# Kernel tuning notes

Measured on AMD Instinct MI355X. Metric: run time of the kernel, lower is better.

Reference implementation:

```python
import jax, jax.numpy as jnp
import numpy as np

N_NODES = 50000
N_EDGES = 600000
D_IN = 128
D_HID = 128


def _gcn_layer(x, src, dst, W, b, n):
    # PyG GCNConv: h = x @ W; add self-loops; symmetric normalization
    # out_i = sum_j (d_i^-1/2 d_j^-1/2) h_j + (d_i^-1) h_i + b, with d = deg + 1
    h = x @ W  # [N, F]
    ones = jnp.ones(src.shape[0], dtype=x.dtype)
    deg = jax.ops.segment_sum(ones, dst, num_segments=n) + jnp.asarray(1.0, x.dtype)
    dinv = jax.lax.rsqrt(deg)  # [N]
    coef = dinv[src] * dinv[dst]  # [E]
    msg = h[src] * coef[:, None]  # gather + scale, [E, F]
    agg = jax.ops.segment_sum(msg, dst, num_segments=n)  # scatter-add, [N, F]
    agg = agg + h * (dinv * dinv)[:, None]  # self-loop contribution
    return agg + b


def setup_inputs() -> dict:
    key = jax.random.key(0)
    k1, k2, k3, k4 = jax.random.split(key, 4)
    x = jax.random.normal(k1, (N_NODES, D_IN), dtype=jnp.float32)
    edge_index = jax.random.randint(k2, (2, N_EDGES), 0, N_NODES, dtype=jnp.int32)
    # Glorot-ish init for linear weights
    W1 = jax.random.normal(k3, (D_IN, D_HID), dtype=jnp.float32) / np.sqrt(D_IN)
    W2 = jax.random.normal(k4, (D_HID, D_HID), dtype=jnp.float32) / np.sqrt(D_HID)
    b1 = jnp.zeros((D_HID,), dtype=jnp.float32)
    b2 = jnp.zeros((D_HID,), dtype=jnp.float32)
    return {"x": x, "edge_index": edge_index, "W1": W1, "b1": b1, "W2": W2, "b2": b2}


def reference(x, edge_index, W1, b1, W2, b2):
    src = edge_index[0]
    dst = edge_index[1]
    n = x.shape[0]
    h = _gcn_layer(x, src, dst, W1, b1, n)
    h = jax.nn.relu(h)
    out = _gcn_layer(h, src, dst, W2, b2, n)
    return out
```

## Files before the change

### kernel.cpp

```cpp
#include <hip/hip_runtime.h>
#include <hip/hip_bf16.h>

typedef __attribute__((ext_vector_type(8))) short short8;
typedef __attribute__((ext_vector_type(4))) float floatx4;

#define D 128
#define BCAP 2048
#define CPAD 16

__device__ __forceinline__ unsigned short f2bf(float f) {
    unsigned u = __float_as_uint(f);
    u += 0x7FFFu + ((u >> 16) & 1u);
    return (unsigned short)(u >> 16);
}
__device__ __forceinline__ float bf2f(unsigned short h) {
    return __uint_as_float(((unsigned)h) << 16);
}
__device__ __forceinline__ float bflo(unsigned p) { return __uint_as_float(p << 16); }
__device__ __forceinline__ float bfhi(unsigned p) { return __uint_as_float(p & 0xFFFF0000u); }

__global__ __launch_bounds__(256) void bucket_wconv_kernel(const int* __restrict__ src,
                                                           const int* __restrict__ dst,
                                                           int* __restrict__ bcnt,
                                                           unsigned* __restrict__ bucket, int E,
                                                           const float* __restrict__ W1,
                                                           const float* __restrict__ W2,
                                                           unsigned short* __restrict__ whi1,
                                                           unsigned short* __restrict__ wlo1,
                                                           unsigned short* __restrict__ whi2,
                                                           unsigned short* __restrict__ wlo2,
                                                           int eb4) {
    int b = blockIdx.x;
    if (b >= eb4) {
        int gid = (b - eb4) * 256 + threadIdx.x;
        int which = gid >> 14;
        int tid = gid & 16383;
        const float* W = which ? W2 : W1;
        unsigned short* whi = which ? whi2 : whi1;
        unsigned short* wlo = which ? wlo2 : wlo1;
        int j    = tid & 7;
        int col  = (tid >> 3) & 127;
        int quad = (tid >> 10) & 3;
        int kb   = tid >> 12;
        float wv = W[(kb * 32 + quad * 8 + j) * D + col];
        unsigned u = __float_as_uint(wv);
        unsigned short h = (unsigned short)(u >> 16);
        whi[tid] = h;
        wlo[tid] = f2bf(wv - bf2f(h));
        return;
    }
    int sub = b & 7;
    int t4 = (b * 256 + threadIdx.x) * 4;
    if (t4 + 3 < E) {
        int4 s = *reinterpret_cast<const int4*>(src + t4);
        int4 d = *reinterpret_cast<const int4*>(dst + t4);
        #pragma unroll
        for (int k = 0; k < 4; k++) {
            int dd = (k == 0) ? d.x : (k == 1) ? d.y : (k == 2) ? d.z : d.w;
            int ss = (k == 0) ? s.x : (k == 1) ? s.y : (k == 2) ? s.z : s.w;
            int slot = ((dd >> 8) << 3) | sub;
            int pos = atomicAdd(&bcnt[slot * CPAD], 1);
            if (pos < BCAP)
                bucket[(size_t)slot * BCAP + pos] = ((unsigned)(dd & 255) << 16) | (unsigned)ss;
        }
    } else {
        for (int i = t4; i < E; i++) {
            int dd = dst[i], ss = src[i];
            int slot = ((dd >> 8) << 3) | sub;
            int pos = atomicAdd(&bcnt[slot * CPAD], 1);
            if (pos < BCAP)
                bucket[(size_t)slot * BCAP + pos] = ((unsigned)(dd & 255) << 16) | (unsigned)ss;
        }
    }
}

__device__ __forceinline__ int block_excl_scan256(int v, int* lds, int tid) {
    int lane = tid & 63, wid = tid >> 6;
    int x = v;
    #pragma unroll
    for (int d = 1; d < 64; d <<= 1) {
        int y = __shfl_up(x, d, 64);
        if (lane >= d) x += y;
    }
    if (lane == 63) lds[wid] = x;
    __syncthreads();
    if (tid == 0) {
        int run = 0;
        #pragma unroll
        for (int i = 0; i < 4; i++) { int t2 = lds[i]; lds[i] = run; run += t2; }
    }
    __syncthreads();
    return lds[wid] + x - v;
}

__global__ __launch_bounds__(256) void build_gemm_kernel(const unsigned* __restrict__ bucket,
                                                         const int* __restrict__ bcnt,
                                                         int* __restrict__ row_ptr,
                                                         float* __restrict__ dinv,
                                                         int* __restrict__ esrc, int N, int E,
                                                         const float* __restrict__ A,
                                                         const unsigned short* __restrict__ whi,
                                                         const unsigned short* __restrict__ wlo,
                                                         unsigned short* __restrict__ C, int M,
                                                         int nbuk) {
    __shared__ int lds4[4];
    __shared__ int sbase[256];
    __shared__ int hist[256];
    __shared__ int cur[256];
    int tid = threadIdx.x;
    int b = blockIdx.x;
    if (b < nbuk) {
        int tot = 0;
        if (tid < nbuk) {
            #pragma unroll
            for (int s = 0; s < 8; s++) tot += min(bcnt[(tid * 8 + s) * CPAD], BCAP);
        }
        int ex = block_excl_scan256(tot, lds4, tid);
        sbase[tid] = ex;
        hist[tid] = 0;
        __syncthreads();
        int base = sbase[b];
        for (int sub = 0; sub < 8; sub++) {
            int cnt = min(bcnt[(b * 8 + sub) * CPAD], BCAP);
            const unsigned* bp = bucket + (size_t)(b * 8 + sub) * BCAP;
            for (int i = tid; i < cnt; i += 256)
                atomicAdd(&hist[bp[i] >> 16], 1);
        }
        __syncthreads();
        int h = hist[tid];
        int off = block_excl_scan256(h, lds4, tid);
        cur[tid] = base + off;
        int node = b * 256 + tid;
        if (node < N) {
            row_ptr[node] = base + off;
            dinv[node] = rsqrtf((float)(h + 1));
        }
        if (b == 0 && tid == 0) row_ptr[N] = E;
        __syncthreads();
        for (int sub = 0; sub < 8; sub++) {
            int cnt = min(bcnt[(b * 8 + sub) * CPAD], BCAP);
            const unsigned* bp = bucket + (size_t)(b * 8 + sub) * BCAP;
            for (int i = tid; i < cnt; i += 256) {
                unsigned v = bp[i];
                int p = atomicAdd(&cur[v >> 16], 1);
                esrc[p] = (int)(v & 0xFFFFu);
            }
        }
        return;
    }
    int lane = tid & 63, wid = tid >> 6;
    int quad = lane >> 4, l15 = lane & 15;
    int row0 = (b - nbuk) * 64;
    int n0 = wid * 32;

    short8 bhi[2][4], blo[2][4];
    #pragma unroll
    for (int t = 0; t < 2; t++)
        #pragma unroll
        for (int kb = 0; kb < 4; kb++) {
            size_t base = ((size_t)((kb * 4 + quad) * 128 + (n0 + t * 16 + l15))) * 8;
            bhi[t][kb] = *reinterpret_cast<const short8*>(whi + base);
            blo[t][kb] = *reinterpret_cast<const short8*>(wlo + base);
        }

    #pragma unroll
    for (int rg = 0; rg < 4; rg++) {
        int r0 = row0 + rg * 16;
        int ar = r0 + l15; if (ar > M - 1) ar = M - 1;
        short8 ahi[4], alo[4];
        #pragma unroll
        for (int kb = 0; kb < 4; kb++) {
            const float4* ap = reinterpret_cast<const float4*>(A + (size_t)ar * D + kb * 32 + quad * 8);
            float4 v0 = ap[0], v1 = ap[1];
            float vv[8] = {v0.x, v0.y, v0.z, v0.w, v1.x, v1.y, v1.z, v1.w};
            short8 vh, vl;
            #pragma unroll
            for (int j = 0; j < 8; j++) {
                unsigned u = __float_as_uint(vv[j]);
                unsigned short h = (unsigned short)(u >> 16);
                vh[j] = (short)h;
                vl[j] = (short)f2bf(vv[j] - bf2f(h));
            }
            ahi[kb] = vh;
            alo[kb] = vl;
        }
        floatx4 acc0 = {0.f, 0.f, 0.f, 0.f};
        floatx4 acc1 = {0.f, 0.f, 0.f, 0.f};
        #pragma unroll
        for (int kb = 0; kb < 4; kb++) {
            acc0 = __builtin_amdgcn_mfma_f32_16x16x32_bf16(ahi[kb], bhi[0][kb], acc0, 0, 0, 0);
            acc1 = __builtin_amdgcn_mfma_f32_16x16x32_bf16(ahi[kb], bhi[1][kb], acc1, 0, 0, 0);
            acc0 = __builtin_amdgcn_mfma_f32_16x16x32_bf16(ahi[kb], blo[0][kb], acc0, 0, 0, 0);
            acc1 = __builtin_amdgcn_mfma_f32_16x16x32_bf16(ahi[kb], blo[1][kb], acc1, 0, 0, 0);
            acc0 = __builtin_amdgcn_mfma_f32_16x16x32_bf16(alo[kb], bhi[0][kb], acc0, 0, 0, 0);
            acc1 = __builtin_amdgcn_mfma_f32_16x16x32_bf16(alo[kb], bhi[1][kb], acc1, 0, 0, 0);
        }
        #pragma unroll
        for (int r = 0; r < 4; r++) {
            int orow = r0 + quad * 4 + r;
            if (orow < M) {
                C[(size_t)orow * D + n0 + l15]      = f2bf(acc0[r]);
                C[(size_t)orow * D + n0 + 16 + l15] = f2bf(acc1[r]);
            }
        }
    }
}

__device__ __forceinline__ void agg_qbody(const uint4* __restrict__ H4,
                                          const float* __restrict__ dinv,
                                          const int* __restrict__ row_ptr,
                                          const int* __restrict__ esrc,
                                          const float* __restrict__ bias,
                                          int node, int fl, float* acc) {
    #pragma unroll
    for (int j = 0; j < 8; j++) acc[j] = 0.f;
    int beg = row_ptr[node], end = row_ptr[node + 1];
    int e = beg;
    for (; e + 4 <= end; e += 4) {
        int s0 = esrc[e], s1 = esrc[e + 1], s2 = esrc[e + 2], s3 = esrc[e + 3];
        float c0 = dinv[s0], c1 = dinv[s1], c2 = dinv[s2], c3 = dinv[s3];
        uint4 p0 = H4[(size_t)s0 * 16 + fl];
        uint4 p1 = H4[(size_t)s1 * 16 + fl];
        uint4 p2 = H4[(size_t)s2 * 16 + fl];
        uint4 p3 = H4[(size_t)s3 * 16 + fl];
        acc[0] += c0 * bflo(p0.x) + c1 * bflo(p1.x) + c2 * bflo(p2.x) + c3 * bflo(p3.x);
        acc[1] += c0 * bfhi(p0.x) + c1 * bfhi(p1.x) + c2 * bfhi(p2.x) + c3 * bfhi(p3.x);
        acc[2] += c0 * bflo(p0.y) + c1 * bflo(p1.y) + c2 * bflo(p2.y) + c3 * bflo(p3.y);
        acc[3] += c0 * bfhi(p0.y) + c1 * bfhi(p1.y) + c2 * bfhi(p2.y) + c3 * bfhi(p3.y);
        acc[4] += c0 * bflo(p0.z) + c1 * bflo(p1.z) + c2 * bflo(p2.z) + c3 * bflo(p3.z);
        acc[5] += c0 * bfhi(p0.z) + c1 * bfhi(p1.z) + c2 * bfhi(p2.z) + c3 * bfhi(p3.z);
        acc[6] += c0 * bflo(p0.w) + c1 * bflo(p1.w) + c2 * bflo(p2.w) + c3 * bflo(p3.w);
        acc[7] += c0 * bfhi(p0.w) + c1 * bfhi(p1.w) + c2 * bfhi(p2.w) + c3 * bfhi(p3.w);
    }
    for (; e < end; e++) {
        int s0 = esrc[e];
        float c = dinv[s0];
        uint4 p0 = H4[(size_t)s0 * 16 + fl];
        acc[0] += c * bflo(p0.x); acc[1] += c * bfhi(p0.x);
        acc[2] += c * bflo(p0.y); acc[3] += c * bfhi(p0.y);
        acc[4] += c * bflo(p0.z); acc[5] += c * bfhi(p0.z);
        acc[6] += c * bflo(p0.w); acc[7] += c * bfhi(p0.w);
    }
    float di = dinv[node];
    float dii = di * di;
    uint4 ps = H4[(size_t)node * 16 + fl];
    const float4* b4 = (const float4*)bias;
    float4 bb0 = b4[fl * 2], bb1 = b4[fl * 2 + 1];
    #pragma unroll
    for (int j = 0; j < 8; j++) acc[j] *= di;
    acc[0] += dii * bflo(ps.x) + bb0.x;
    acc[1] += dii * bfhi(ps.x) + bb0.y;
    acc[2] += dii * bflo(ps.y) + bb0.z;
    acc[3] += dii * bfhi(ps.y) + bb0.w;
    acc[4] += dii * bflo(ps.z) + bb1.x;
    acc[5] += dii * bfhi(ps.z) + bb1.y;
    acc[6] += dii * bflo(ps.w) + bb1.z;
    acc[7] += dii * bfhi(ps.w) + bb1.w;
}

__global__ __launch_bounds__(256) void agg_gemm2_kernel(const unsigned short* __restrict__ H,
                                                        const float* __restrict__ dinv,
                                                        const int* __restrict__ row_ptr,
                                                        const int* __restrict__ esrc,
                                                        const float* __restrict__ bias,
                                                        const unsigned short* __restrict__ whi,
                                                        const unsigned short* __restrict__ wlo,
                                                        unsigned short* __restrict__ C, int N) {
    __shared__ unsigned short Asm[16 * 136];
    int tid = threadIdx.x;
    int node0 = blockIdx.x * 16;
    int r = tid >> 4;
    int fl = tid & 15;
    int node = node0 + r;
    float acc[8];
    if (node < N) {
        agg_qbody((const uint4*)H, dinv, row_ptr, esrc, bias, node, fl, acc);
    } else {
        #pragma unroll
        for (int j = 0; j < 8; j++) acc[j] = 0.f;
    }
    short8 a;
    #pragma unroll
    for (int j = 0; j < 8; j++) a[j] = (short)f2bf(fmaxf(acc[j], 0.f));
    *reinterpret_cast<short8*>(&Asm[r * 136 + fl * 8]) = a;
    __syncthreads();

    int lane = tid & 63, wid = tid >> 6;
    int quad = lane >> 4, l15 = lane & 15;
    int n0 = wid * 32;
    floatx4 acc0 = {0.f, 0.f, 0.f, 0.f};
    floatx4 acc1 = {0.f, 0.f, 0.f, 0.f};
    #pragma unroll 1
    for (int kb = 0; kb < 4; kb++) {
        size_t wb = ((size_t)((kb * 4 + quad) * 128 + (n0 + l15))) * 8;
        short8 bh0 = *reinterpret_cast<const short8*>(whi + wb);
        short8 bh1 = *reinterpret_cast<const short8*>(whi + wb + 128);
        short8 bl0 = *reinterpret_cast<const short8*>(wlo + wb);
        short8 bl1 = *reinterpret_cast<const short8*>(wlo + wb + 128);
        short8 af = *reinterpret_cast<const short8*>(&Asm[l15 * 136 + kb * 32 + quad * 8]);
        acc0 = __builtin_amdgcn_mfma_f32_16x16x32_bf16(af, bh0, acc0, 0, 0, 0);
        acc1 = __builtin_amdgcn_mfma_f32_16x16x32_bf16(af, bh1, acc1, 0, 0, 0);
        acc0 = __builtin_amdgcn_mfma_f32_16x16x32_bf16(af, bl0, acc0, 0, 0, 0);
        acc1 = __builtin_amdgcn_mfma_f32_16x16x32_bf16(af, bl1, acc1, 0, 0, 0);
    }
    #pragma unroll
    for (int rr = 0; rr < 4; rr++) {
        int orow = node0 + quad * 4 + rr;
        if (orow < N) {
            C[(size_t)orow * D + n0 + l15]      = f2bf(acc0[rr]);
            C[(size_t)orow * D + n0 + 16 + l15] = f2bf(acc1[rr]);
        }
    }
}

__global__ __launch_bounds__(256) void agg_f32out_kernel(const unsigned short* __restrict__ H,
                                                         const float* __restrict__ dinv,
                                                         const int* __restrict__ row_ptr,
                                                         const int* __restrict__ esrc,
                                                         const float* __restrict__ bias,
                                                         float4* __restrict__ out, int N) {
    int node = blockIdx.x * 16 + (threadIdx.x >> 4);
    int fl = threadIdx.x & 15;
    if (node >= N) return;
    float acc[8];
    agg_qbody((const uint4*)H, dinv, row_ptr, esrc, bias, node, fl, acc);
    float4 o0, o1;
    o0.x = acc[0]; o0.y = acc[1]; o0.z = acc[2]; o0.w = acc[3];
    o1.x = acc[4]; o1.y = acc[5]; o1.z = acc[6]; o1.w = acc[7];
    out[(size_t)node * 32 + fl * 2]     = o0;
    out[(size_t)node * 32 + fl * 2 + 1] = o1;
}

extern "C" void kernel_launch(void* const* d_in, const int* in_sizes, int n_in,
                              void* d_out, int out_size, void* d_ws, size_t ws_size,
                              hipStream_t stream) {
    const float* x  = (const float*)d_in[0];
    const int*   ei = (const int*)d_in[1];
    const float* W1 = (const float*)d_in[2];
    const float* b1 = (const float*)d_in[3];
    const float* W2 = (const float*)d_in[4];
    const float* b2 = (const float*)d_in[5];

    int N = in_sizes[0] / D;
    int E = in_sizes[1] / 2;
    const int* src = ei;
    const int* dst = ei + E;

    int nbuk = (N + 255) / 256;

    char* ws = (char*)d_ws;
    int*      bcnt   = (int*)(ws + 0);
    unsigned* bucket = (unsigned*)(ws + 102400);
    int*      row_ptr= (int*)(ws + 12947456);
    float*    dinv   = (float*)(ws + 13147520);
    int*      esrcs  = (int*)(ws + 13347520);
    unsigned short* whi1 = (unsigned short*)(ws + 15747584);
    unsigned short* wlo1 = (unsigned short*)(ws + 15780352);
    unsigned short* whi2 = (unsigned short*)(ws + 15813120);
    unsigned short* wlo2 = (unsigned short*)(ws + 15845888);
    unsigned short* hfeat = (unsigned short*)(ws + 15878656);
    unsigned short* h2    = (unsigned short*)(ws + 28678656);

    int eb4  = (E / 4 + 255) / 256;
    int gb   = (N + 63) / 64;
    int ab16 = (N + 15) / 16;

    hipMemsetAsync(bcnt, 0, (size_t)nbuk * 8 * CPAD * sizeof(int), stream);
    bucket_wconv_kernel<<<eb4 + 128, 256, 0, stream>>>(src, dst, bcnt, bucket, E,
                                                       W1, W2, whi1, wlo1, whi2, wlo2, eb4);

    build_gemm_kernel<<<nbuk + gb, 256, 0, stream>>>(bucket, bcnt, row_ptr, dinv, esrcs,
                                                     N, E, x, whi1, wlo1, hfeat, N, nbuk);

    agg_gemm2_kernel<<<ab16, 256, 0, stream>>>(hfeat, dinv, row_ptr, esrcs, b1,
                                               whi2, wlo2, h2, N);

    agg_f32out_kernel<<<ab16, 256, 0, stream>>>(h2, dinv, row_ptr, esrcs, b2,
                                                (float4*)d_out, N);
}
```

Baseline: 192.4 us.

## Compute degrees in bucketing pass and pack source coefficient into CSR edges

Per-node in-degrees are now counted with global atomics during edge bucketing, replacing the LDS histogram pass over buckets in the CSR build. The CSR edge array becomes (src, dinv[src]) pairs, so the aggregation kernels no longer do a dependent gather of dinv per edge. The aggregation inner loop is also unrolled to 8 edges to keep more feature loads in flight. The cost is an extra global atomic per edge, a random deg read per edge during the build, and a doubled edge array footprint.

```diff
diff --git a/kernel.cpp b/kernel.cpp
--- a/kernel.cpp
+++ b/kernel.cpp
@@ -22,6 +22,7 @@
 __global__ __launch_bounds__(256) void bucket_wconv_kernel(const int* __restrict__ src,
                                                            const int* __restrict__ dst,
                                                            int* __restrict__ bcnt,
+                                                           int* __restrict__ deg,
                                                            unsigned* __restrict__ bucket, int E,
                                                            const float* __restrict__ W1,
                                                            const float* __restrict__ W2,
@@ -59,6 +60,7 @@
             int dd = (k == 0) ? d.x : (k == 1) ? d.y : (k == 2) ? d.z : d.w;
             int ss = (k == 0) ? s.x : (k == 1) ? s.y : (k == 2) ? s.z : s.w;
             int slot = ((dd >> 8) << 3) | sub;
+            atomicAdd(&deg[dd], 1);
             int pos = atomicAdd(&bcnt[slot * CPAD], 1);
             if (pos < BCAP)
                 bucket[(size_t)slot * BCAP + pos] = ((unsigned)(dd & 255) << 16) | (unsigned)ss;
@@ -67,6 +69,7 @@
         for (int i = t4; i < E; i++) {
             int dd = dst[i], ss = src[i];
             int slot = ((dd >> 8) << 3) | sub;
+            atomicAdd(&deg[dd], 1);
             int pos = atomicAdd(&bcnt[slot * CPAD], 1);
             if (pos < BCAP)
                 bucket[(size_t)slot * BCAP + pos] = ((unsigned)(dd & 255) << 16) | (unsigned)ss;
@@ -95,9 +98,10 @@
 
 __global__ __launch_bounds__(256) void build_gemm_kernel(const unsigned* __restrict__ bucket,
                                                          const int* __restrict__ bcnt,
+                                                         const int* __restrict__ deg,
                                                          int* __restrict__ row_ptr,
                                                          float* __restrict__ dinv,
-                                                         int* __restrict__ esrc, int N, int E,
+                                                         uint2* __restrict__ edata, int N, int E,
                                                          const float* __restrict__ A,
                                                          const unsigned short* __restrict__ whi,
                                                          const unsigned short* __restrict__ wlo,
@@ -105,7 +109,6 @@
                                                          int nbuk) {
     __shared__ int lds4[4];
     __shared__ int sbase[256];
-    __shared__ int hist[256];
     __shared__ int cur[256];
     int tid = threadIdx.x;
     int b = blockIdx.x;
@@ -117,20 +120,12 @@
         }
         int ex = block_excl_scan256(tot, lds4, tid);
         sbase[tid] = ex;
-        hist[tid] = 0;
         __syncthreads();
         int base = sbase[b];
-        for (int sub = 0; sub < 8; sub++) {
-            int cnt = min(bcnt[(b * 8 + sub) * CPAD], BCAP);
-            const unsigned* bp = bucket + (size_t)(b * 8 + sub) * BCAP;
-            for (int i = tid; i < cnt; i += 256)
-                atomicAdd(&hist[bp[i] >> 16], 1);
-        }
-        __syncthreads();
-        int h = hist[tid];
+        int node = b * 256 + tid;
+        int h = (node < N) ? deg[node] : 0;
         int off = block_excl_scan256(h, lds4, tid);
         cur[tid] = base + off;
-        int node = b * 256 + tid;
         if (node < N) {
             row_ptr[node] = base + off;
             dinv[node] = rsqrtf((float)(h + 1));
@@ -142,8 +137,11 @@
             const unsigned* bp = bucket + (size_t)(b * 8 + sub) * BCAP;
             for (int i = tid; i < cnt; i += 256) {
                 unsigned v = bp[i];
+                int ss = (int)(v & 0xFFFFu);
                 int p = atomicAdd(&cur[v >> 16], 1);
-                esrc[p] = (int)(v & 0xFFFFu);
+                float cs = rsqrtf((float)(deg[ss] + 1));
+                uint2 ent; ent.x = (unsigned)ss; ent.y = __float_as_uint(cs);
+                edata[p] = ent;
             }
         }
         return;
@@ -206,36 +204,59 @@
     }
 }
 
+#define ACC4(c0, p0, c1, p1, c2, p2, c3, p3) \
+    acc[0] += c0 * bflo(p0.x) + c1 * bflo(p1.x) + c2 * bflo(p2.x) + c3 * bflo(p3.x); \
+    acc[1] += c0 * bfhi(p0.x) + c1 * bfhi(p1.x) + c2 * bfhi(p2.x) + c3 * bfhi(p3.x); \
+    acc[2] += c0 * bflo(p0.y) + c1 * bflo(p1.y) + c2 * bflo(p2.y) + c3 * bflo(p3.y); \
+    acc[3] += c0 * bfhi(p0.y) + c1 * bfhi(p1.y) + c2 * bfhi(p2.y) + c3 * bfhi(p3.y); \
+    acc[4] += c0 * bflo(p0.z) + c1 * bflo(p1.z) + c2 * bflo(p2.z) + c3 * bflo(p3.z); \
+    acc[5] += c0 * bfhi(p0.z) + c1 * bfhi(p1.z) + c2 * bfhi(p2.z) + c3 * bfhi(p3.z); \
+    acc[6] += c0 * bflo(p0.w) + c1 * bflo(p1.w) + c2 * bflo(p2.w) + c3 * bflo(p3.w); \
+    acc[7] += c0 * bfhi(p0.w) + c1 * bfhi(p1.w) + c2 * bfhi(p2.w) + c3 * bfhi(p3.w);
+
 __device__ __forceinline__ void agg_qbody(const uint4* __restrict__ H4,
+                                          const uint2* __restrict__ ed,
                                           const float* __restrict__ dinv,
                                           const int* __restrict__ row_ptr,
-                                          const int* __restrict__ esrc,
                                           const float* __restrict__ bias,
                                           int node, int fl, float* acc) {
     #pragma unroll
     for (int j = 0; j < 8; j++) acc[j] = 0.f;
     int beg = row_ptr[node], end = row_ptr[node + 1];
     int e = beg;
-    for (; e + 4 <= end; e += 4) {
-        int s0 = esrc[e], s1 = esrc[e + 1], s2 = esrc[e + 2], s3 = esrc[e + 3];
-        float c0 = dinv[s0], c1 = dinv[s1], c2 = dinv[s2], c3 = dinv[s3];
-        uint4 p0 = H4[(size_t)s0 * 16 + fl];
-        uint4 p1 = H4[(size_t)s1 * 16 + fl];
-        uint4 p2 = H4[(size_t)s2 * 16 + fl];
-        uint4 p3 = H4[(size_t)s3 * 16 + fl];
-        acc[0] += c0 * bflo(p0.x) + c1 * bflo(p1.x) + c2 * bflo(p2.x) + c3 * bflo(p3.x);
-        acc[1] += c0 * bfhi(p0.x) + c1 * bfhi(p1.x) + c2 * bfhi(p2.x) + c3 * bfhi(p3.x);
-        acc[2] += c0 * bflo(p0.y) + c1 * bflo(p1.y) + c2 * bflo(p2.y) + c3 * bflo(p3.y);
-        acc[3] += c0 * bfhi(p0.y) + c1 * bfhi(p1.y) + c2 * bfhi(p2.y) + c3 * bfhi(p3.y);
-        acc[4] += c0 * bflo(p0.z) + c1 * bflo(p1.z) + c2 * bflo(p2.z) + c3 * bflo(p3.z);
-        acc[5] += c0 * bfhi(p0.z) + c1 * bfhi(p1.z) + c2 * bfhi(p2.z) + c3 * bfhi(p3.z);
-        acc[6] += c0 * bflo(p0.w) + c1 * bflo(p1.w) + c2 * bflo(p2.w) + c3 * bflo(p3.w);
-        acc[7] += c0 * bfhi(p0.w) + c1 * bfhi(p1.w) + c2 * bfhi(p2.w) + c3 * bfhi(p3.w);
+    for (; e + 8 <= end; e += 8) {
+        uint2 q0 = ed[e],     q1 = ed[e + 1], q2 = ed[e + 2], q3 = ed[e + 3];
+        uint2 q4 = ed[e + 4], q5 = ed[e + 5], q6 = ed[e + 6], q7 = ed[e + 7];
+        uint4 p0 = H4[(size_t)q0.x * 16 + fl];
+        uint4 p1 = H4[(size_t)q1.x * 16 + fl];
+        uint4 p2 = H4[(size_t)q2.x * 16 + fl];
+        uint4 p3 = H4[(size_t)q3.x * 16 + fl];
+        uint4 p4 = H4[(size_t)q4.x * 16 + fl];
+        uint4 p5 = H4[(size_t)q5.x * 16 + fl];
+        uint4 p6 = H4[(size_t)q6.x * 16 + fl];
+        uint4 p7 = H4[(size_t)q7.x * 16 + fl];
+        float c0 = __uint_as_float(q0.y), c1 = __uint_as_float(q1.y);
+        float c2 = __uint_as_float(q2.y), c3 = __uint_as_float(q3.y);
+        float c4 = __uint_as_float(q4.y), c5 = __uint_as_float(q5.y);
+        float c6 = __uint_as_float(q6.y), c7 = __uint_as_float(q7.y);
+        ACC4(c0, p0, c1, p1, c2, p2, c3, p3);
+        ACC4(c4, p4, c5, p5, c6, p6, c7, p7);
+    }
+    if (e + 4 <= end) {
+        uint2 q0 = ed[e], q1 = ed[e + 1], q2 = ed[e + 2], q3 = ed[e + 3];
+        uint4 p0 = H4[(size_t)q0.x * 16 + fl];
+        uint4 p1 = H4[(size_t)q1.x * 16 + fl];
+        uint4 p2 = H4[(size_t)q2.x * 16 + fl];
+        uint4 p3 = H4[(size_t)q3.x * 16 + fl];
+        float c0 = __uint_as_float(q0.y), c1 = __uint_as_float(q1.y);
+        float c2 = __uint_as_float(q2.y), c3 = __uint_as_float(q3.y);
+        ACC4(c0, p0, c1, p1, c2, p2, c3, p3);
+        e += 4;
     }
     for (; e < end; e++) {
-        int s0 = esrc[e];
-        float c = dinv[s0];
-        uint4 p0 = H4[(size_t)s0 * 16 + fl];
+        uint2 q0 = ed[e];
+        float c = __uint_as_float(q0.y);
+        uint4 p0 = H4[(size_t)q0.x * 16 + fl];
         acc[0] += c * bflo(p0.x); acc[1] += c * bfhi(p0.x);
         acc[2] += c * bflo(p0.y); acc[3] += c * bfhi(p0.y);
         acc[4] += c * bflo(p0.z); acc[5] += c * bfhi(p0.z);
@@ -259,9 +280,9 @@
 }
 
 __global__ __launch_bounds__(256) void agg_gemm2_kernel(const unsigned short* __restrict__ H,
+                                                        const uint2* __restrict__ ed,
                                                         const float* __restrict__ dinv,
                                                         const int* __restrict__ row_ptr,
-                                                        const int* __restrict__ esrc,
                                                         const float* __restrict__ bias,
                                                         const unsigned short* __restrict__ whi,
                                                         const unsigned short* __restrict__ wlo,
@@ -274,7 +295,7 @@
     int node = node0 + r;
     float acc[8];
     if (node < N) {
-        agg_qbody((const uint4*)H, dinv, row_ptr, esrc, bias, node, fl, acc);
+        agg_qbody((const uint4*)H, ed, dinv, row_ptr, bias, node, fl, acc);
     } else {
         #pragma unroll
         for (int j = 0; j < 8; j++) acc[j] = 0.f;
@@ -314,16 +335,16 @@
 }
 
 __global__ __launch_bounds__(256) void agg_f32out_kernel(const unsigned short* __restrict__ H,
+                                                         const uint2* __restrict__ ed,
                                                          const float* __restrict__ dinv,
                                                          const int* __restrict__ row_ptr,
-                                                         const int* __restrict__ esrc,
                                                          const float* __restrict__ bias,
                                                          float4* __restrict__ out, int N) {
     int node = blockIdx.x * 16 + (threadIdx.x >> 4);
     int fl = threadIdx.x & 15;
     if (node >= N) return;
     float acc[8];
-    agg_qbody((const uint4*)H, dinv, row_ptr, esrc, bias, node, fl, acc);
+    agg_qbody((const uint4*)H, ed, dinv, row_ptr, bias, node, fl, acc);
     float4 o0, o1;
     o0.x = acc[0]; o0.y = acc[1]; o0.z = acc[2]; o0.w = acc[3];
     o1.x = acc[4]; o1.y = acc[5]; o1.z = acc[6]; o1.w = acc[7];
@@ -350,31 +371,32 @@
 
     char* ws = (char*)d_ws;
     int*      bcnt   = (int*)(ws + 0);
-    unsigned* bucket = (unsigned*)(ws + 102400);
-    int*      row_ptr= (int*)(ws + 12947456);
-    float*    dinv   = (float*)(ws + 13147520);
-    int*      esrcs  = (int*)(ws + 13347520);
-    unsigned short* whi1 = (unsigned short*)(ws + 15747584);
-    unsigned short* wlo1 = (unsigned short*)(ws + 15780352);
-    unsigned short* whi2 = (unsigned short*)(ws + 15813120);
-    unsigned short* wlo2 = (unsigned short*)(ws + 15845888);
-    unsigned short* hfeat = (unsigned short*)(ws + 15878656);
-    unsigned short* h2    = (unsigned short*)(ws + 28678656);
+    int*      deg    = (int*)(ws + 102400);
+    unsigned* bucket = (unsigned*)(ws + 307200);
+    int*      row_ptr= (int*)(ws + 13152256);
+    float*    dinv   = (float*)(ws + 13357056);
+    uint2*    edata  = (uint2*)(ws + 13561856);
+    unsigned short* whi1 = (unsigned short*)(ws + 18366464);
+    unsigned short* wlo1 = (unsigned short*)(ws + 18399232);
+    unsigned short* whi2 = (unsigned short*)(ws + 18432000);
+    unsigned short* wlo2 = (unsigned short*)(ws + 18464768);
+    unsigned short* hfeat = (unsigned short*)(ws + 18497536);
+    unsigned short* h2    = (unsigned short*)(ws + 31297536);
 
     int eb4  = (E / 4 + 255) / 256;
     int gb   = (N + 63) / 64;
     int ab16 = (N + 15) / 16;
 
-    hipMemsetAsync(bcnt, 0, (size_t)nbuk * 8 * CPAD * sizeof(int), stream);
-    bucket_wconv_kernel<<<eb4 + 128, 256, 0, stream>>>(src, dst, bcnt, bucket, E,
+    hipMemsetAsync(bcnt, 0, 307200, stream);
+    bucket_wconv_kernel<<<eb4 + 128, 256, 0, stream>>>(src, dst, bcnt, deg, bucket, E,
                                                        W1, W2, whi1, wlo1, whi2, wlo2, eb4);
 
-    build_gemm_kernel<<<nbuk + gb, 256, 0, stream>>>(bucket, bcnt, row_ptr, dinv, esrcs,
+    build_gemm_kernel<<<nbuk + gb, 256, 0, stream>>>(bucket, bcnt, deg, row_ptr, dinv, edata,
                                                      N, E, x, whi1, wlo1, hfeat, N, nbuk);
 
-    agg_gemm2_kernel<<<ab16, 256, 0, stream>>>(hfeat, dinv, row_ptr, esrcs, b1,
+    agg_gemm2_kernel<<<ab16, 256, 0, stream>>>(hfeat, edata, dinv, row_ptr, b1,
                                                whi2, wlo2, h2, N);
 
-    agg_f32out_kernel<<<ab16, 256, 0, stream>>>(h2, dinv, row_ptr, esrcs, b2,
+    agg_f32out_kernel<<<ab16, 256, 0, stream>>>(h2, edata, dinv, row_ptr, b2,
                                                 (float4*)d_out, N);
 }
```

Measured after the change: 222.8 us. 15.8% more time.

## Bin edges locally in LDS before scattering into global buckets

Applied to the files above, without the earlier changes.

The edge-bucketing pass now uses 256 blocks that each take a contiguous chunk of edges. Each block builds a shared-memory histogram by destination bucket and does a counting sort in LDS. It then reserves space with one global atomic per bucket and writes the sorted entries out. This replaces one global atomic per edge and scattered writes with aggregated atomics and more contiguous stores, at the cost of large LDS use and fewer blocks.

```diff
diff --git a/kernel.cpp b/kernel.cpp
--- a/kernel.cpp
+++ b/kernel.cpp
@@ -7,6 +7,8 @@
 #define D 128
 #define BCAP 2048
 #define CPAD 16
+#define NBIN 256
+#define EPBMAX 2560
 
 __device__ __forceinline__ unsigned short f2bf(float f) {
     unsigned u = __float_as_uint(f);
@@ -18,6 +20,25 @@
 }
 __device__ __forceinline__ float bflo(unsigned p) { return __uint_as_float(p << 16); }
 __device__ __forceinline__ float bfhi(unsigned p) { return __uint_as_float(p & 0xFFFF0000u); }
+
+__device__ __forceinline__ int block_excl_scan256(int v, int* lds, int tid) {
+    int lane = tid & 63, wid = tid >> 6;
+    int x = v;
+    #pragma unroll
+    for (int d = 1; d < 64; d <<= 1) {
+        int y = __shfl_up(x, d, 64);
+        if (lane >= d) x += y;
+    }
+    if (lane == 63) lds[wid] = x;
+    __syncthreads();
+    if (tid == 0) {
+        int run = 0;
+        #pragma unroll
+        for (int i = 0; i < 4; i++) { int t2 = lds[i]; lds[i] = run; run += t2; }
+    }
+    __syncthreads();
+    return lds[wid] + x - v;
+}
 
 __global__ __launch_bounds__(256) void bucket_wconv_kernel(const int* __restrict__ src,
                                                            const int* __restrict__ dst,
@@ -29,10 +50,10 @@
                                                            unsigned short* __restrict__ wlo1,
                                                            unsigned short* __restrict__ whi2,
                                                            unsigned short* __restrict__ wlo2,
-                                                           int eb4) {
+                                                           int nbuk) {
     int b = blockIdx.x;
-    if (b >= eb4) {
-        int gid = (b - eb4) * 256 + threadIdx.x;
+    if (b >= NBIN) {
+        int gid = (b - NBIN) * 256 + threadIdx.x;
         int which = gid >> 14;
         int tid = gid & 16383;
         const float* W = which ? W2 : W1;
@@ -49,48 +70,57 @@
         wlo[tid] = f2bf(wv - bf2f(h));
         return;
     }
+    __shared__ unsigned lent[EPBMAX];
+    __shared__ unsigned sorted_e[EPBMAX];
+    __shared__ int sdst[EPBMAX];
+    __shared__ unsigned short loff[EPBMAX];
+    __shared__ unsigned char lbkt[EPBMAX];
+    __shared__ int hist[256];
+    __shared__ int lstart[256];
+    __shared__ int gbase[256];
+    __shared__ int lds4[4];
+
+    int tid = threadIdx.x;
     int sub = b & 7;
-    int t4 = (b * 256 + threadIdx.x) * 4;
-    if (t4 + 3 < E) {
-        int4 s = *reinterpret_cast<const int4*>(src + t4);
-        int4 d = *reinterpret_cast<const int4*>(dst + t4);
-        #pragma unroll
-        for (int k = 0; k < 4; k++) {
-            int dd = (k == 0) ? d.x : (k == 1) ? d.y : (k == 2) ? d.z : d.w;
-            int ss = (k == 0) ? s.x : (k == 1) ? s.y : (k == 2) ? s.z : s.w;
-            int slot = ((dd >> 8) << 3) | sub;
-            int pos = atomicAdd(&bcnt[slot * CPAD], 1);
-            if (pos < BCAP)
-                bucket[(size_t)slot * BCAP + pos] = ((unsigned)(dd & 255) << 16) | (unsigned)ss;
-        }
-    } else {
-        for (int i = t4; i < E; i++) {
-            int dd = dst[i], ss = src[i];
-            int slot = ((dd >> 8) << 3) | sub;
-            int pos = atomicAdd(&bcnt[slot * CPAD], 1);
-            if (pos < BCAP)
-                bucket[(size_t)slot * BCAP + pos] = ((unsigned)(dd & 255) << 16) | (unsigned)ss;
-        }
-    }
-}
-
-__device__ __forceinline__ int block_excl_scan256(int v, int* lds, int tid) {
-    int lane = tid & 63, wid = tid >> 6;
-    int x = v;
-    #pragma unroll
-    for (int d = 1; d < 64; d <<= 1) {
-        int y = __shfl_up(x, d, 64);
-        if (lane >= d) x += y;
-    }
-    if (lane == 63) lds[wid] = x;
-    __syncthreads();
-    if (tid == 0) {
-        int run = 0;
-        #pragma unroll
-        for (int i = 0; i < 4; i++) { int t2 = lds[i]; lds[i] = run; run += t2; }
-    }
-    __syncthreads();
-    return lds[wid] + x - v;
+    int epb = (E + NBIN - 1) / NBIN;
+    int beg = b * epb;
+    int cnt = E - beg;
+    if (cnt > epb) cnt = epb;
+    if (cnt < 0) cnt = 0;
+
+    hist[tid] = 0;
+    __syncthreads();
+
+    for (int i = tid; i < cnt; i += 256) {
+        int dd = dst[beg + i], ss = src[beg + i];
+        int bk = dd >> 8;
+        lent[i] = ((unsigned)(dd & 255) << 16) | (unsigned)ss;
+        lbkt[i] = (unsigned char)bk;
+        loff[i] = (unsigned short)atomicAdd(&hist[bk], 1);
+    }
+    __syncthreads();
+
+    int h = hist[tid];
+    int ex = block_excl_scan256(h, lds4, tid);
+    lstart[tid] = ex;
+    if (tid < nbuk && h > 0)
+        gbase[tid] = atomicAdd(&bcnt[(tid * 8 + sub) * CPAD], h);
+    __syncthreads();
+
+    for (int i = tid; i < cnt; i += 256) {
+        int bk = lbkt[i];
+        int of = loff[i];
+        int lp = lstart[bk] + of;
+        int gp = gbase[bk] + of;
+        sorted_e[lp] = lent[i];
+        sdst[lp] = (gp < BCAP) ? ((bk * 8 + sub) * BCAP + gp) : -1;
+    }
+    __syncthreads();
+
+    for (int i = tid; i < cnt; i += 256) {
+        int dsti = sdst[i];
+        if (dsti >= 0) bucket[dsti] = sorted_e[i];
+    }
 }
 
 __global__ __launch_bounds__(256) void build_gemm_kernel(const unsigned* __restrict__ bucket,
@@ -361,13 +391,12 @@
     unsigned short* hfeat = (unsigned short*)(ws + 15878656);
     unsigned short* h2    = (unsigned short*)(ws + 28678656);
 
-    int eb4  = (E / 4 + 255) / 256;
     int gb   = (N + 63) / 64;
     int ab16 = (N + 15) / 16;
 
-    hipMemsetAsync(bcnt, 0, (size_t)nbuk * 8 * CPAD * sizeof(int), stream);
-    bucket_wconv_kernel<<<eb4 + 128, 256, 0, stream>>>(src, dst, bcnt, bucket, E,
-                                                       W1, W2, whi1, wlo1, whi2, wlo2, eb4);
+    hipMemsetAsync(bcnt, 0, 102400, stream);
+    bucket_wconv_kernel<<<NBIN + 128, 256, 0, stream>>>(src, dst, bcnt, bucket, E,
+                                                        W1, W2, whi1, wlo1, whi2, wlo2, nbuk);
 
     build_gemm_kernel<<<nbuk + gb, 256, 0, stream>>>(bucket, bcnt, row_ptr, dinv, esrcs,
                                                      N, E, x, whi1, wlo1, hfeat, N, nbuk);
```

Measured after the change: 168.0 us. 12.7% less time.
